# Performance work log

Measured on AMD Instinct MI355X. Metric: run time of the kernel, lower is better.

The kernel has to match this reference:

```python
import jax, jax.numpy as jnp
import numpy as np
import math

N_HEAD = 16
D_MODEL = 1024
KSIZE = 3
PAD = 1


def _conv1d(x, w, b, pad):
    # x: [B, C_in, S], w: [C_out, C_in, K] (torch Conv1d layout)
    y = jax.lax.conv_general_dilated(
        x, w, window_strides=(1,), padding=[(pad, pad)],
        dimension_numbers=("NCH", "OIH", "NCH"))
    return y + b[None, :, None]


def setup_inputs() -> dict:
    key = jax.random.key(0)
    ks = jax.random.split(key, 10)
    B, S, D = 2, 2048, D_MODEL
    sc = 1.0 / math.sqrt(D)
    return {
        "q": jax.random.normal(ks[0], (B, S, D), jnp.float32),
        "k": jax.random.normal(ks[1], (B, S, D), jnp.float32),
        "v": jax.random.normal(ks[2], (B, S, D), jnp.float32),
        "wq_w": jax.random.normal(ks[3], (D, D, KSIZE), jnp.float32) * sc,
        "wq_b": jnp.zeros((D,), jnp.float32),
        "wk_w": jax.random.normal(ks[4], (D, D, KSIZE), jnp.float32) * sc,
        "wk_b": jnp.zeros((D,), jnp.float32),
        "wv_w": jax.random.normal(ks[5], (D, D, 1), jnp.float32) * sc,
        "wv_b": jnp.zeros((D,), jnp.float32),
        "wc_w": jax.random.normal(ks[6], (D, D), jnp.float32) * sc,
        "wc_b": jnp.zeros((D,), jnp.float32),
    }


def reference(q, k, v, wq_w, wq_b, wk_w, wk_b, wv_w, wv_b, wc_w, wc_b):
    B, S, D = q.shape
    h = N_HEAD
    d = D // h
    # channels-first for conv projections: [B, D, S]
    qc = _conv1d(jnp.swapaxes(q, 1, 2), wq_w, wq_b, PAD)
    kc = _conv1d(jnp.swapaxes(k, 1, 2), wk_w, wk_b, PAD)
    vc = _conv1d(jnp.swapaxes(v, 1, 2), wv_w, wv_b, 0)
    # faithful to torch: view(b, d, h, s) then transpose(1,2).transpose(2,3) -> [b, h, s, d]
    # (head index is the FAST axis of the channel dim, matching the original)
    qh = jnp.transpose(qc.reshape(B, d, h, S), (0, 2, 3, 1))
    kh = jnp.transpose(kc.reshape(B, d, h, S), (0, 2, 3, 1))
    vh = jnp.transpose(vc.reshape(B, d, h, S), (0, 2, 3, 1))
    scores = jnp.einsum("bhqd,bhkd->bhqk", qh, kh) / math.sqrt(d)
    attn = jax.nn.softmax(scores, axis=-1)
    out = jnp.einsum("bhqk,bhkd->bhqd", attn, vh)
    # concat: [b,h,s,d] -> [b,s,h*d]
    out = jnp.transpose(out, (0, 2, 1, 3)).reshape(B, S, D)
    # torch Linear: x @ W^T + b
    return out @ wc_w.T + wc_b
```

## Files before the change

### kernel.cpp

```cpp
#include <hip/hip_runtime.h>
#include <hip/hip_bf16.h>

#define SS 2048
#define DDIM 1024

typedef unsigned short u16;
typedef unsigned int u32;
typedef __attribute__((ext_vector_type(8))) short bf16x8_t;
typedef __attribute__((ext_vector_type(4))) float f32x4_t;

__device__ __forceinline__ u16 f2bf(float f) {
  __hip_bfloat16 h = __float2bfloat16(f);
  return *reinterpret_cast<u16*>(&h);
}

__device__ __forceinline__ void gld16(const void* g, void* lds_base) {
  __builtin_amdgcn_global_load_lds(
      (const __attribute__((address_space(1))) u32*)(uintptr_t)g,
      (__attribute__((address_space(3))) u32*)(u32)(uintptr_t)lds_base,
      16, 0, 0);
}

__global__ void zero_kernel(u32* zb) { zb[threadIdx.x] = 0u; }

__global__ __launch_bounds__(256) void convert3_kernel(
    const float* __restrict__ q, const float* __restrict__ k,
    const float* __restrict__ v, u16* __restrict__ Xq, u16* __restrict__ Xk,
    u16* __restrict__ Xv) {
  const int z = blockIdx.y;
  const float* src = (z == 0) ? q : (z == 1) ? k : v;
  u16* dst = (z == 0) ? Xq : (z == 1) ? Xk : Xv;
  int i = blockIdx.x * 256 + threadIdx.x;
  const float4* s = (const float4*)src + (size_t)i * 2;
  float4 f0 = s[0], f1 = s[1];
  u16 o[8] = {f2bf(f0.x), f2bf(f0.y), f2bf(f0.z), f2bf(f0.w),
              f2bf(f1.x), f2bf(f1.y), f2bf(f1.z), f2bf(f1.w)};
  *(uint4*)(dst + (size_t)i * 8) = *(const uint4*)o;
}

__global__ __launch_bounds__(256) void repack3_kernel(
    const float* __restrict__ wq, const float* __restrict__ wk,
    u16* __restrict__ Wqr, u16* __restrict__ Wkr) {
  const float* w = blockIdx.y ? wk : wq;
  u16* out = blockIdx.y ? Wkr : Wqr;
  int o = blockIdx.x;
  for (int j = threadIdx.x; j < 3072; j += 256) {
    int i = j / 3, t = j - i * 3;
    out[(size_t)o * 3072 + t * 1024 + i] = f2bf(w[(size_t)o * 3072 + j]);
  }
}

__global__ __launch_bounds__(256) void repackc_kernel(
    const float* __restrict__ wv, const float* __restrict__ wc,
    u16* __restrict__ Wvr, u16* __restrict__ Wcr) {
  const float* w = blockIdx.y ? wc : wv;
  u16* out = blockIdx.y ? Wcr : Wvr;
  size_t i = (size_t)blockIdx.x * 1024 + threadIdx.x * 4;
  float4 f = *(const float4*)(w + i);
  u16 o4[4] = {f2bf(f.x), f2bf(f.y), f2bf(f.z), f2bf(f.w)};
  *(ushort4*)(out + i) = *(const ushort4*)o4;
}

__global__ __launch_bounds__(256) void mfma_proj(
    const u16* __restrict__ Xq, const u16* __restrict__ Xk,
    const u16* __restrict__ Xv, const u16* __restrict__ Wq,
    const u16* __restrict__ Wk, const u16* __restrict__ Wv,
    const float* __restrict__ bq, const float* __restrict__ bk,
    const float* __restrict__ bv, u16* __restrict__ Qhb,
    u16* __restrict__ Khb, u16* __restrict__ Vtb,
    const u16* __restrict__ zbuf) {
  __shared__ __attribute__((aligned(16))) u16 As2[2][128][40];
  __shared__ __attribute__((aligned(16))) u16 Bs2[2][128][40];
  const int z = blockIdx.z;
  const u16* __restrict__ Xb = (z == 0) ? Xq : (z == 1) ? Xk : Xv;
  const u16* __restrict__ Wr = (z == 0) ? Wq : (z == 1) ? Wk : Wv;
  const float* __restrict__ bias = (z == 0) ? bq : (z == 1) ? bk : bv;
  u16* __restrict__ Cptr = (z == 0) ? Qhb : (z == 1) ? Khb : Vtb;
  const int nk = (z == 2) ? 32 : 96;
  const bool conv = (z < 2);
  const bool vout = (z == 2);
  const float scale = (z == 0) ? 0.125f : 1.0f;
  const int Kdim = (z == 2) ? 1024 : 3072;

  const int tid = threadIdx.x;
  const int lane = tid & 63;
  const int w = tid >> 6;
  const int ln = tid & 15;
  const int quad = (tid >> 4) & 3;
  const int wrow = w >> 1, wcol = w & 1;
  const int m0 = blockIdx.x * 128, n0 = blockIdx.y * 128;

  const char* p[5];
  int dinc[5];
  u32 ldso[5];
  bool act[5], isA[5], loA[5], hiA[5];
  const char* pbaseA[5];

#pragma unroll
  for (int i = 0; i < 5; ++i) {
    int c = w + 4 * i;
    isA[i] = (c < 10);
    if (c < 10) {
      int G = c * 64 + lane;
      int x = G / 5, kb = G - x * 5;
      int gm = m0 + x;
      int b = gm >> 11, s = gm & 2047;
      act[i] = (kb < 4);
      ldso[i] = c * 1024;
      const char* pb = (const char*)(Xb + (size_t)(b * SS + s) * DDIM + kb * 8);
      pbaseA[i] = pb;
      loA[i] = (s == 0);
      hiA[i] = (s == 2047);
      if (conv) {
        p[i] = loA[i] ? (const char*)zbuf : (pb - 2048);
        dinc[i] = loA[i] ? 0 : 64;
      } else {
        p[i] = pb;
        dinc[i] = 64;
      }
    } else {
      int c2 = c - 10;
      int G = c2 * 64 + lane;
      int x = G / 5, kb = G - x * 5;
      act[i] = (kb < 4);
      ldso[i] = c2 * 1024;
      p[i] = (const char*)(Wr + (size_t)(n0 + x) * Kdim + kb * 8);
      dinc[i] = 64;
      pbaseA[i] = nullptr;
      loA[i] = hiA[i] = false;
    }
  }

  auto stage = [&](int bi) {
#pragma unroll
    for (int i = 0; i < 5; ++i) {
      char* dst = (isA[i] ? (char*)As2[bi] : (char*)Bs2[bi]) + ldso[i];
      if (act[i]) gld16(p[i], dst);
      p[i] += dinc[i];
    }
  };

  f32x4_t acc[4][4];
#pragma unroll
  for (int i = 0; i < 4; ++i)
#pragma unroll
    for (int j = 0; j < 4; ++j) acc[i][j] = (f32x4_t){0.f, 0.f, 0.f, 0.f};

  stage(0);
  stage(1);

#pragma unroll 2
  for (int ks = 0; ks < nk; ++ks) {
    const int cur = ks & 1;
    if (ks + 1 < nk)
      asm volatile("s_waitcnt vmcnt(5)\ns_barrier" ::: "memory");
    else
      asm volatile("s_waitcnt vmcnt(0)\ns_barrier" ::: "memory");

    const u16(*As)[40] = As2[cur];
    const u16(*Bs)[40] = Bs2[cur];
    bf16x8_t a[4], b[4];
#pragma unroll
    for (int mt = 0; mt < 4; ++mt)
      a[mt] = *(const bf16x8_t*)&As[wrow * 64 + mt * 16 + ln][quad * 8];
#pragma unroll
    for (int nt = 0; nt < 4; ++nt)
      b[nt] = *(const bf16x8_t*)&Bs[wcol * 64 + nt * 16 + ln][quad * 8];
    asm volatile("s_waitcnt lgkmcnt(0)\ns_barrier" ::: "memory");

    const int j = ks + 2;
    if (j < nk) {
      if (conv && (j & 31) == 0) {
#pragma unroll
        for (int i = 0; i < 5; ++i) {
          if (isA[i]) {
            if (j == 32) {
              if (loA[i]) { p[i] = pbaseA[i]; dinc[i] = 64; }
            } else {
              if (hiA[i]) { p[i] = (const char*)zbuf; dinc[i] = 0; }
            }
          }
        }
      }
      stage(cur);
    }

    __builtin_amdgcn_s_setprio(1);
#pragma unroll
    for (int mt = 0; mt < 4; ++mt)
#pragma unroll
      for (int nt = 0; nt < 4; ++nt)
        acc[mt][nt] = __builtin_amdgcn_mfma_f32_16x16x32_bf16(
            a[mt], b[nt], acc[mt][nt], 0, 0, 0);
    __builtin_amdgcn_s_setprio(0);
  }

#pragma unroll
  for (int mt = 0; mt < 4; ++mt) {
#pragma unroll
    for (int nt = 0; nt < 4; ++nt) {
      int gn = n0 + wcol * 64 + nt * 16 + ln;
      float bi = bias[gn];
#pragma unroll
      for (int r = 0; r < 4; ++r) {
        int gm = m0 + wrow * 64 + mt * 16 + quad * 4 + r;
        float val = (acc[mt][nt][r] + bi) * scale;
        int b = gm >> 11, s = gm & 2047;
        int hh = gn & 15, dd = gn >> 4;
        if (!vout)
          Cptr[((size_t)(b * 16 + hh) * SS + s) * 64 + dd] = f2bf(val);
        else
          Cptr[((size_t)(b * 16 + hh) * 64 + dd) * SS + s] = f2bf(val);
      }
    }
  }
}

__global__ __launch_bounds__(256) void mfma_gemm_lin(
    const u16* __restrict__ Xb, const u16* __restrict__ Wr,
    const float* __restrict__ bias, float* __restrict__ Cptr) {
  __shared__ __attribute__((aligned(16))) u16 As2[2][32][40];
  __shared__ __attribute__((aligned(16))) u16 Bs2[2][128][40];
  const int tid = threadIdx.x;
  const int lane = tid & 63;
  const int w = tid >> 6;
  const int ln = tid & 15;
  const int quad = (tid >> 4) & 3;
  const int wrow = w >> 1, wcol = w & 1;
  const int m0 = blockIdx.x * 32, n0 = blockIdx.y * 128;

  const char* p[4];
  u32 ldso[4];
  bool ok[4], act[4], isA[4];
#pragma unroll
  for (int i = 0; i < 4; ++i) {
    int c = w + 4 * i;
    ok[i] = (c < 13);
    if (c < 3) {
      int G = c * 64 + lane;
      int x = G / 5, kb = G - x * 5;
      isA[i] = true;
      act[i] = (kb < 4) && (x < 32);
      ldso[i] = c * 1024;
      p[i] = (const char*)(Xb + (size_t)(m0 + x) * DDIM + kb * 8);
    } else if (c < 13) {
      int c2 = c - 3;
      int G = c2 * 64 + lane;
      int x = G / 5, kb = G - x * 5;
      isA[i] = false;
      act[i] = (kb < 4);
      ldso[i] = c2 * 1024;
      p[i] = (const char*)(Wr + (size_t)(n0 + x) * 1024 + kb * 8);
    } else {
      isA[i] = false; act[i] = false; ldso[i] = 0; p[i] = nullptr;
    }
  }

  auto stage = [&](int bi) {
#pragma unroll
    for (int i = 0; i < 4; ++i) {
      if (ok[i]) {
        char* dst = (isA[i] ? (char*)As2[bi] : (char*)Bs2[bi]) + ldso[i];
        if (act[i]) gld16(p[i], dst);
        p[i] += 64;
      }
    }
  };

  f32x4_t acc[4];
#pragma unroll
  for (int j = 0; j < 4; ++j) acc[j] = (f32x4_t){0.f, 0.f, 0.f, 0.f};

  stage(0);
  stage(1);

#pragma unroll 2
  for (int ks = 0; ks < 32; ++ks) {
    const int cur = ks & 1;
    if (ks + 1 < 32) {
      if (w == 0) asm volatile("s_waitcnt vmcnt(4)\ns_barrier" ::: "memory");
      else        asm volatile("s_waitcnt vmcnt(3)\ns_barrier" ::: "memory");
    } else {
      asm volatile("s_waitcnt vmcnt(0)\ns_barrier" ::: "memory");
    }

    const u16(*As)[40] = As2[cur];
    const u16(*Bs)[40] = Bs2[cur];
    bf16x8_t a = *(const bf16x8_t*)&As[wrow * 16 + ln][quad * 8];
    bf16x8_t b[4];
#pragma unroll
    for (int nt = 0; nt < 4; ++nt)
      b[nt] = *(const bf16x8_t*)&Bs[wcol * 64 + nt * 16 + ln][quad * 8];
    asm volatile("s_waitcnt lgkmcnt(0)\ns_barrier" ::: "memory");

    if (ks + 2 < 32) stage(cur);

    __builtin_amdgcn_s_setprio(1);
#pragma unroll
    for (int nt = 0; nt < 4; ++nt)
      acc[nt] = __builtin_amdgcn_mfma_f32_16x16x32_bf16(a, b[nt], acc[nt], 0, 0, 0);
    __builtin_amdgcn_s_setprio(0);
  }

#pragma unroll
  for (int nt = 0; nt < 4; ++nt) {
    int gn = n0 + wcol * 64 + nt * 16 + ln;
    float bi = bias[gn];
#pragma unroll
    for (int r = 0; r < 4; ++r) {
      int gm = m0 + wrow * 16 + quad * 4 + r;
      Cptr[(size_t)gm * DDIM + gn] = acc[nt][r] + bi;
    }
  }
}

__global__ __launch_bounds__(256) void mfma_attn(
    const u16* __restrict__ Qhb, const u16* __restrict__ Khb,
    const u16* __restrict__ Vtb, u16* __restrict__ Aob,
    const u16* __restrict__ zbuf) {
  __shared__ __attribute__((aligned(16))) u16 Ks2[2][64][72];
  __shared__ __attribute__((aligned(16))) u16 Vt2[2][64][72];
  __shared__ __attribute__((aligned(16))) u16 Ps[4][16][72];
  const int tid = threadIdx.x;
  const int lane = tid & 63;
  const int w = tid >> 6;
  const int ln = tid & 15;
  const int quad = (tid >> 4) & 3;
  const int bh = blockIdx.y;
  const int b = bh >> 4, hh = bh & 15;
  const int s0 = blockIdx.x * 64;

  const char* p[5];
  int dinc[5];
  u32 ldso[5];
  bool ok[5], act[5], isK[5];
#pragma unroll
  for (int i = 0; i < 5; ++i) {
    int c = w + 4 * i;
    ok[i] = (c < 18);
    if (c < 9) {
      int G = c * 64 + lane;
      int x = G / 9, db = G - x * 9;
      isK[i] = true;
      act[i] = (db < 8);
      ldso[i] = c * 1024;
      p[i] = (const char*)(Khb + ((size_t)bh * SS + x) * 64 + db * 8);
      dinc[i] = 8192;
    } else if (c < 18) {
      int c2 = c - 9;
      int G = c2 * 64 + lane;
      int x = G / 9, db = G - x * 9;
      isK[i] = false;
      act[i] = (db < 8);
      ldso[i] = c2 * 1024;
      p[i] = (const char*)(Vtb + ((size_t)bh * 64 + x) * SS + db * 8);
      dinc[i] = 128;
    } else {
      isK[i] = false; ok[i] = false; act[i] = false; ldso[i] = 0;
      p[i] = nullptr; dinc[i] = 0;
    }
  }

  auto stage = [&](int bi) {
#pragma unroll
    for (int i = 0; i < 5; ++i) {
      if (ok[i]) {
        char* dst = (isK[i] ? (char*)Ks2[bi] : (char*)Vt2[bi]) + ldso[i];
        if (act[i]) gld16(p[i], dst);
        p[i] += dinc[i];
      }
    }
  };

  const u16* qp = Qhb + ((size_t)bh * SS + s0 + w * 16 + ln) * 64 + quad * 8;
  bf16x8_t qf0 = *(const bf16x8_t*)qp;
  bf16x8_t qf1 = *(const bf16x8_t*)(qp + 32);

  float mrow[4], lsum[4];
  f32x4_t oacc[4];
#pragma unroll
  for (int r = 0; r < 4; ++r) { mrow[r] = -3e38f; lsum[r] = 0.f; }
#pragma unroll
  for (int dt = 0; dt < 4; ++dt) oacc[dt] = (f32x4_t){0.f, 0.f, 0.f, 0.f};

  stage(0);
  stage(1);

#pragma unroll 2
  for (int kt = 0; kt < 32; ++kt) {
    const int cur = kt & 1;
    if (kt + 1 < 32) {
      if (w < 2) asm volatile("s_waitcnt vmcnt(5)\ns_barrier" ::: "memory");
      else       asm volatile("s_waitcnt vmcnt(4)\ns_barrier" ::: "memory");
    } else {
      asm volatile("s_waitcnt vmcnt(0)\ns_barrier" ::: "memory");
    }

    const u16(*Ks)[72] = Ks2[cur];
    const u16(*Vt)[72] = Vt2[cur];

    f32x4_t sc[4];
#pragma unroll
    for (int nt = 0; nt < 4; ++nt) sc[nt] = (f32x4_t){0.f, 0.f, 0.f, 0.f};
    __builtin_amdgcn_s_setprio(1);
#pragma unroll
    for (int nt = 0; nt < 4; ++nt) {
      bf16x8_t k0f = *(const bf16x8_t*)&Ks[nt * 16 + ln][quad * 8];
      sc[nt] = __builtin_amdgcn_mfma_f32_16x16x32_bf16(qf0, k0f, sc[nt], 0, 0, 0);
      bf16x8_t k1f = *(const bf16x8_t*)&Ks[nt * 16 + ln][32 + quad * 8];
      sc[nt] = __builtin_amdgcn_mfma_f32_16x16x32_bf16(qf1, k1f, sc[nt], 0, 0, 0);
    }
    __builtin_amdgcn_s_setprio(0);

    float mxv[4];
    bool need = false;
#pragma unroll
    for (int r = 0; r < 4; ++r) {
      float mx = fmaxf(fmaxf(sc[0][r], sc[1][r]), fmaxf(sc[2][r], sc[3][r]));
      mx = fmaxf(mx, __shfl_xor(mx, 1, 64));
      mx = fmaxf(mx, __shfl_xor(mx, 2, 64));
      mx = fmaxf(mx, __shfl_xor(mx, 4, 64));
      mx = fmaxf(mx, __shfl_xor(mx, 8, 64));
      mxv[r] = mx;
      need = need || (mx > mrow[r]);
    }
    if (__any(need)) {
#pragma unroll
      for (int r = 0; r < 4; ++r) {
        float mn = fmaxf(mrow[r], mxv[r]);
        float al = __expf(mrow[r] - mn);
        mrow[r] = mn;
        lsum[r] *= al;
#pragma unroll
        for (int dt = 0; dt < 4; ++dt) oacc[dt][r] *= al;
      }
    }
#pragma unroll
    for (int r = 0; r < 4; ++r) {
      float p0 = __expf(sc[0][r] - mrow[r]), p1 = __expf(sc[1][r] - mrow[r]);
      float p2 = __expf(sc[2][r] - mrow[r]), p3 = __expf(sc[3][r] - mrow[r]);
      lsum[r] += p0 + p1 + p2 + p3;
      Ps[w][quad * 4 + r][ln] = f2bf(p0);
      Ps[w][quad * 4 + r][16 + ln] = f2bf(p1);
      Ps[w][quad * 4 + r][32 + ln] = f2bf(p2);
      Ps[w][quad * 4 + r][48 + ln] = f2bf(p3);
    }

    bf16x8_t pa0 = *(const bf16x8_t*)&Ps[w][ln][quad * 8];
    bf16x8_t pa1 = *(const bf16x8_t*)&Ps[w][ln][32 + quad * 8];
    __builtin_amdgcn_s_setprio(1);
#pragma unroll
    for (int dt = 0; dt < 4; ++dt) {
      bf16x8_t v0f = *(const bf16x8_t*)&Vt[dt * 16 + ln][quad * 8];
      oacc[dt] = __builtin_amdgcn_mfma_f32_16x16x32_bf16(pa0, v0f, oacc[dt], 0, 0, 0);
      bf16x8_t v1f = *(const bf16x8_t*)&Vt[dt * 16 + ln][32 + quad * 8];
      oacc[dt] = __builtin_amdgcn_mfma_f32_16x16x32_bf16(pa1, v1f, oacc[dt], 0, 0, 0);
    }
    __builtin_amdgcn_s_setprio(0);

    asm volatile("s_waitcnt lgkmcnt(0)\ns_barrier" ::: "memory");
    if (kt + 2 < 32) stage(cur);
  }

  float inv[4];
#pragma unroll
  for (int r = 0; r < 4; ++r) {
    float t = lsum[r];
    t += __shfl_xor(t, 1, 64);
    t += __shfl_xor(t, 2, 64);
    t += __shfl_xor(t, 4, 64);
    t += __shfl_xor(t, 8, 64);
    inv[r] = 1.f / t;
  }
#pragma unroll
  for (int dt = 0; dt < 4; ++dt)
#pragma unroll
    for (int r = 0; r < 4; ++r) {
      int gm = b * SS + s0 + w * 16 + quad * 4 + r;
      Aob[(size_t)gm * DDIM + hh * 64 + dt * 16 + ln] = f2bf(oacc[dt][r] * inv[r]);
    }
}

extern "C" void kernel_launch(void* const* d_in, const int* in_sizes, int n_in,
                              void* d_out, int out_size, void* d_ws, size_t ws_size,
                              hipStream_t stream) {
  const float* q    = (const float*)d_in[0];
  const float* k    = (const float*)d_in[1];
  const float* v    = (const float*)d_in[2];
  const float* wq_w = (const float*)d_in[3];
  const float* wq_b = (const float*)d_in[4];
  const float* wk_w = (const float*)d_in[5];
  const float* wk_b = (const float*)d_in[6];
  const float* wv_w = (const float*)d_in[7];
  const float* wv_b = (const float*)d_in[8];
  const float* wc_w = (const float*)d_in[9];
  const float* wc_b = (const float*)d_in[10];

  char* ws = (char*)d_ws;
  size_t off = 0;
  u16* zbuf = (u16*)(ws + off); off += 256;
  const size_t SZ_ACT = (size_t)2 * SS * DDIM * 2;
  u16* Xq  = (u16*)(ws + off); off += SZ_ACT;
  u16* Xk  = (u16*)(ws + off); off += SZ_ACT;
  u16* Xv  = (u16*)(ws + off); off += SZ_ACT;
  u16* Wqr = (u16*)(ws + off); off += (size_t)1024 * 3072 * 2;
  u16* Wkr = (u16*)(ws + off); off += (size_t)1024 * 3072 * 2;
  u16* Wvr = (u16*)(ws + off); off += (size_t)1024 * 1024 * 2;
  u16* Wcr = (u16*)(ws + off); off += (size_t)1024 * 1024 * 2;
  u16* Qhb = (u16*)(ws + off); off += SZ_ACT;
  u16* Khb = (u16*)(ws + off); off += SZ_ACT;
  u16* Vtb = (u16*)(ws + off); off += SZ_ACT;
  u16* Aob = (u16*)(ws + off); off += SZ_ACT;
  if (ws_size < off) return;

  zero_kernel<<<1, 64, 0, stream>>>((u32*)zbuf);
  convert3_kernel<<<dim3(2048, 3), 256, 0, stream>>>(q, k, v, Xq, Xk, Xv);
  repack3_kernel<<<dim3(1024, 2), 256, 0, stream>>>(wq_w, wk_w, Wqr, Wkr);
  repackc_kernel<<<dim3(1024, 2), 256, 0, stream>>>(wv_w, wc_w, Wvr, Wcr);

  mfma_proj<<<dim3(32, 8, 3), 256, 0, stream>>>(
      Xq, Xk, Xv, Wqr, Wkr, Wvr, wq_b, wk_b, wv_b, Qhb, Khb, Vtb, zbuf);

  mfma_attn<<<dim3(32, 32), 256, 0, stream>>>(Qhb, Khb, Vtb, Aob, zbuf);

  mfma_gemm_lin<<<dim3(128, 8), 256, 0, stream>>>(Aob, Wcr, wc_b, (float*)d_out);
}
```

Baseline: 393.1 us.

## Fuse prep kernels, reorder MFMA before barrier, use wave-wide softmax max

Merges the zero, input-convert and two weight-repack launches into a single prep kernel to cut launch overhead. In the projection and linear GEMMs, the MFMA block now issues before the LDS-drain barrier, with a sched_barrier, so compute overlaps the next stage's loads. In attention, the per-row running max is replaced by one wave-wide max shared by all rows, removing the __any vote and per-row rescales. A shared max across 16 query rows can underflow exp for rows whose scores sit far below the wave max, which risks accuracy.

```diff
diff --git a/kernel.cpp b/kernel.cpp
--- a/kernel.cpp
+++ b/kernel.cpp
@@ -21,44 +21,48 @@
       16, 0, 0);
 }
 
-__global__ void zero_kernel(u32* zb) { zb[threadIdx.x] = 0u; }
-
-__global__ __launch_bounds__(256) void convert3_kernel(
+__global__ __launch_bounds__(256) void prep_kernel(
     const float* __restrict__ q, const float* __restrict__ k,
-    const float* __restrict__ v, u16* __restrict__ Xq, u16* __restrict__ Xk,
-    u16* __restrict__ Xv) {
-  const int z = blockIdx.y;
-  const float* src = (z == 0) ? q : (z == 1) ? k : v;
-  u16* dst = (z == 0) ? Xq : (z == 1) ? Xk : Xv;
-  int i = blockIdx.x * 256 + threadIdx.x;
-  const float4* s = (const float4*)src + (size_t)i * 2;
-  float4 f0 = s[0], f1 = s[1];
-  u16 o[8] = {f2bf(f0.x), f2bf(f0.y), f2bf(f0.z), f2bf(f0.w),
-              f2bf(f1.x), f2bf(f1.y), f2bf(f1.z), f2bf(f1.w)};
-  *(uint4*)(dst + (size_t)i * 8) = *(const uint4*)o;
-}
-
-__global__ __launch_bounds__(256) void repack3_kernel(
-    const float* __restrict__ wq, const float* __restrict__ wk,
-    u16* __restrict__ Wqr, u16* __restrict__ Wkr) {
-  const float* w = blockIdx.y ? wk : wq;
-  u16* out = blockIdx.y ? Wkr : Wqr;
-  int o = blockIdx.x;
-  for (int j = threadIdx.x; j < 3072; j += 256) {
-    int i = j / 3, t = j - i * 3;
-    out[(size_t)o * 3072 + t * 1024 + i] = f2bf(w[(size_t)o * 3072 + j]);
-  }
-}
-
-__global__ __launch_bounds__(256) void repackc_kernel(
-    const float* __restrict__ wv, const float* __restrict__ wc,
-    u16* __restrict__ Wvr, u16* __restrict__ Wcr) {
-  const float* w = blockIdx.y ? wc : wv;
-  u16* out = blockIdx.y ? Wcr : Wvr;
-  size_t i = (size_t)blockIdx.x * 1024 + threadIdx.x * 4;
-  float4 f = *(const float4*)(w + i);
-  u16 o4[4] = {f2bf(f.x), f2bf(f.y), f2bf(f.z), f2bf(f.w)};
-  *(ushort4*)(out + i) = *(const ushort4*)o4;
+    const float* __restrict__ v, const float* __restrict__ wq_w,
+    const float* __restrict__ wk_w, const float* __restrict__ wv_w,
+    const float* __restrict__ wc_w, u16* __restrict__ Xq,
+    u16* __restrict__ Xk, u16* __restrict__ Xv, u16* __restrict__ Wqr,
+    u16* __restrict__ Wkr, u16* __restrict__ Wvr, u16* __restrict__ Wcr,
+    u32* __restrict__ zbuf) {
+  const int bid = blockIdx.x;
+  const int tid = threadIdx.x;
+  if (bid == 0 && tid < 64) zbuf[tid] = 0u;
+
+  if (bid < 6144) {
+    const int z = bid >> 11;
+    const int bx = bid & 2047;
+    const float* src = (z == 0) ? q : (z == 1) ? k : v;
+    u16* dst = (z == 0) ? Xq : (z == 1) ? Xk : Xv;
+    int i = bx * 256 + tid;
+    const float4* s = (const float4*)src + (size_t)i * 2;
+    float4 f0 = s[0], f1 = s[1];
+    u16 o[8] = {f2bf(f0.x), f2bf(f0.y), f2bf(f0.z), f2bf(f0.w),
+                f2bf(f1.x), f2bf(f1.y), f2bf(f1.z), f2bf(f1.w)};
+    *(uint4*)(dst + (size_t)i * 8) = *(const uint4*)o;
+  } else if (bid < 8192) {
+    const int idx = bid - 6144;
+    const float* w = (idx >= 1024) ? wk_w : wq_w;
+    u16* out = (idx >= 1024) ? Wkr : Wqr;
+    const int o = idx & 1023;
+    for (int j = tid; j < 3072; j += 256) {
+      int i = j / 3, t = j - i * 3;
+      out[(size_t)o * 3072 + t * 1024 + i] = f2bf(w[(size_t)o * 3072 + j]);
+    }
+  } else {
+    const int idx = bid - 8192;
+    const float* w = (idx >= 1024) ? wc_w : wv_w;
+    u16* out = (idx >= 1024) ? Wcr : Wvr;
+    const int bx = idx & 1023;
+    size_t i = (size_t)bx * 1024 + tid * 4;
+    float4 f = *(const float4*)(w + i);
+    u16 o4[4] = {f2bf(f.x), f2bf(f.y), f2bf(f.z), f2bf(f.w)};
+    *(ushort4*)(out + i) = *(const ushort4*)o4;
+  }
 }
 
 __global__ __launch_bounds__(256) void mfma_proj(
@@ -166,7 +170,17 @@
 #pragma unroll
     for (int nt = 0; nt < 4; ++nt)
       b[nt] = *(const bf16x8_t*)&Bs[wcol * 64 + nt * 16 + ln][quad * 8];
+    __builtin_amdgcn_s_setprio(1);
+#pragma unroll
+    for (int mt = 0; mt < 4; ++mt)
+#pragma unroll
+      for (int nt = 0; nt < 4; ++nt)
+        acc[mt][nt] = __builtin_amdgcn_mfma_f32_16x16x32_bf16(
+            a[mt], b[nt], acc[mt][nt], 0, 0, 0);
+    __builtin_amdgcn_s_setprio(0);
+
     asm volatile("s_waitcnt lgkmcnt(0)\ns_barrier" ::: "memory");
+    __builtin_amdgcn_sched_barrier(0);
 
     const int j = ks + 2;
     if (j < nk) {
@@ -184,15 +198,6 @@
       }
       stage(cur);
     }
-
-    __builtin_amdgcn_s_setprio(1);
-#pragma unroll
-    for (int mt = 0; mt < 4; ++mt)
-#pragma unroll
-      for (int nt = 0; nt < 4; ++nt)
-        acc[mt][nt] = __builtin_amdgcn_mfma_f32_16x16x32_bf16(
-            a[mt], b[nt], acc[mt][nt], 0, 0, 0);
-    __builtin_amdgcn_s_setprio(0);
   }
 
 #pragma unroll
@@ -291,15 +296,16 @@
 #pragma unroll
     for (int nt = 0; nt < 4; ++nt)
       b[nt] = *(const bf16x8_t*)&Bs[wcol * 64 + nt * 16 + ln][quad * 8];
-    asm volatile("s_waitcnt lgkmcnt(0)\ns_barrier" ::: "memory");
-
-    if (ks + 2 < 32) stage(cur);
-
     __builtin_amdgcn_s_setprio(1);
 #pragma unroll
     for (int nt = 0; nt < 4; ++nt)
       acc[nt] = __builtin_amdgcn_mfma_f32_16x16x32_bf16(a, b[nt], acc[nt], 0, 0, 0);
     __builtin_amdgcn_s_setprio(0);
+
+    asm volatile("s_waitcnt lgkmcnt(0)\ns_barrier" ::: "memory");
+    __builtin_amdgcn_sched_barrier(0);
+
+    if (ks + 2 < 32) stage(cur);
   }
 
 #pragma unroll
@@ -376,10 +382,11 @@
   bf16x8_t qf0 = *(const bf16x8_t*)qp;
   bf16x8_t qf1 = *(const bf16x8_t*)(qp + 32);
 
-  float mrow[4], lsum[4];
+  float mrow = -3e38f;
+  float lsum[4];
   f32x4_t oacc[4];
 #pragma unroll
-  for (int r = 0; r < 4; ++r) { mrow[r] = -3e38f; lsum[r] = 0.f; }
+  for (int r = 0; r < 4; ++r) lsum[r] = 0.f;
 #pragma unroll
   for (int dt = 0; dt < 4; ++dt) oacc[dt] = (f32x4_t){0.f, 0.f, 0.f, 0.f};
 
@@ -412,33 +419,31 @@
     }
     __builtin_amdgcn_s_setprio(0);
 
-    float mxv[4];
-    bool need = false;
+    float mx = sc[0][0];
+#pragma unroll
+    for (int nt = 0; nt < 4; ++nt)
+#pragma unroll
+      for (int r = 0; r < 4; ++r) mx = fmaxf(mx, sc[nt][r]);
+    mx = fmaxf(mx, __shfl_xor(mx, 1, 64));
+    mx = fmaxf(mx, __shfl_xor(mx, 2, 64));
+    mx = fmaxf(mx, __shfl_xor(mx, 4, 64));
+    mx = fmaxf(mx, __shfl_xor(mx, 8, 64));
+    mx = fmaxf(mx, __shfl_xor(mx, 16, 64));
+    mx = fmaxf(mx, __shfl_xor(mx, 32, 64));
+    if (mx > mrow) {
+      float al = __expf(mrow - mx);
+      mrow = mx;
+#pragma unroll
+      for (int r = 0; r < 4; ++r) lsum[r] *= al;
+#pragma unroll
+      for (int dt = 0; dt < 4; ++dt)
+#pragma unroll
+        for (int r = 0; r < 4; ++r) oacc[dt][r] *= al;
+    }
 #pragma unroll
     for (int r = 0; r < 4; ++r) {
-      float mx = fmaxf(fmaxf(sc[0][r], sc[1][r]), fmaxf(sc[2][r], sc[3][r]));
-      mx = fmaxf(mx, __shfl_xor(mx, 1, 64));
-      mx = fmaxf(mx, __shfl_xor(mx, 2, 64));
-      mx = fmaxf(mx, __shfl_xor(mx, 4, 64));
-      mx = fmaxf(mx, __shfl_xor(mx, 8, 64));
-      mxv[r] = mx;
-      need = need || (mx > mrow[r]);
-    }
-    if (__any(need)) {
-#pragma unroll
-      for (int r = 0; r < 4; ++r) {
-        float mn = fmaxf(mrow[r], mxv[r]);
-        float al = __expf(mrow[r] - mn);
-        mrow[r] = mn;
-        lsum[r] *= al;
-#pragma unroll
-        for (int dt = 0; dt < 4; ++dt) oacc[dt][r] *= al;
-      }
-    }
-#pragma unroll
-    for (int r = 0; r < 4; ++r) {
-      float p0 = __expf(sc[0][r] - mrow[r]), p1 = __expf(sc[1][r] - mrow[r]);
-      float p2 = __expf(sc[2][r] - mrow[r]), p3 = __expf(sc[3][r] - mrow[r]);
+      float p0 = __expf(sc[0][r] - mrow), p1 = __expf(sc[1][r] - mrow);
+      float p2 = __expf(sc[2][r] - mrow), p3 = __expf(sc[3][r] - mrow);
       lsum[r] += p0 + p1 + p2 + p3;
       Ps[w][quad * 4 + r][ln] = f2bf(p0);
       Ps[w][quad * 4 + r][16 + ln] = f2bf(p1);
@@ -459,6 +464,7 @@
     __builtin_amdgcn_s_setprio(0);
 
     asm volatile("s_waitcnt lgkmcnt(0)\ns_barrier" ::: "memory");
+    __builtin_amdgcn_sched_barrier(0);
     if (kt + 2 < 32) stage(cur);
   }
 
@@ -513,10 +519,9 @@
   u16* Aob = (u16*)(ws + off); off += SZ_ACT;
   if (ws_size < off) return;
 
-  zero_kernel<<<1, 64, 0, stream>>>((u32*)zbuf);
-  convert3_kernel<<<dim3(2048, 3), 256, 0, stream>>>(q, k, v, Xq, Xk, Xv);
-  repack3_kernel<<<dim3(1024, 2), 256, 0, stream>>>(wq_w, wk_w, Wqr, Wkr);
-  repackc_kernel<<<dim3(1024, 2), 256, 0, stream>>>(wv_w, wc_w, Wvr, Wcr);
+  prep_kernel<<<10240, 256, 0, stream>>>(q, k, v, wq_w, wk_w, wv_w, wc_w,
+                                         Xq, Xk, Xv, Wqr, Wkr, Wvr, Wcr,
+                                         (u32*)zbuf);
 
   mfma_proj<<<dim3(32, 8, 3), 256, 0, stream>>>(
       Xq, Xk, Xv, Wqr, Wkr, Wvr, wq_b, wk_b, wv_b, Qhb, Khb, Vtb, zbuf);
```

After: 366.1 us. 6.9% less time.
